# Kernel tuning notes

Hardware: AMD Instinct MI355X
Metric: run time of the kernel (lower is better)

## Reference

```python
import jax, jax.numpy as jnp
import numpy as np

N = 8192
FIN = 128
FOUT = 64
NEG_BIG = -9e15


def setup_inputs() -> dict:
    key = jax.random.key(0)
    k1, k2, k3, k4 = jax.random.split(key, 4)
    x = jax.random.normal(k1, (N, FIN), dtype=jnp.float32)
    adj = jax.random.randint(k2, (N, N), 0, 2, dtype=jnp.int32)
    stdv_w = 1.0 / np.sqrt(FOUT)
    W = jax.random.uniform(k3, (FIN, FOUT), dtype=jnp.float32, minval=-stdv_w, maxval=stdv_w)
    # weight2: stdv = 1/sqrt(1) = 1
    a = jax.random.uniform(k4, (2 * FOUT, 1), dtype=jnp.float32, minval=-1.0, maxval=1.0)
    return {"x": x, "adj": adj, "W": W, "a": a}


def reference(x, adj, W, a):
    # h = x W  -> [N, Fout]
    h = x @ W
    # e_ij = relu(a^T [h_i || h_j]) decomposed exactly: a1.h_i + a2.h_j
    a1 = a[:FOUT, 0]  # [Fout]
    a2 = a[FOUT:, 0]  # [Fout]
    s1 = h @ a1  # [N]
    s2 = h @ a2  # [N]
    e = jax.nn.relu(s1[:, None] + s2[None, :])  # [N, N]
    att_logits = jnp.where(adj > 0, e, jnp.float32(NEG_BIG))
    attention = jax.nn.softmax(att_logits, axis=-1)  # [N, N]
    # dropout omitted (eval mode / p applied only in training)
    out = attention @ h  # [N, Fout]
    return out[None]  # [1, N, Fout] matching batch_size=1 reshape
```

## Files before the change

kernel.cpp:

```cpp
#include <hip/hip_runtime.h>
#include <cstdint>
#include <cstddef>

#define NN 8192
#define FIN 128
#define FOUT 64
#define BM 32
#define BN 64
#define JSPLIT 4
#define JCH (NN / JSPLIT)
#define NCHUNK (JCH / BN)
#define LDP 72

typedef __bf16 bf16x8 __attribute__((ext_vector_type(8)));
typedef unsigned short u16x8 __attribute__((ext_vector_type(8)));
typedef float f32x4 __attribute__((ext_vector_type(4)));

__device__ __forceinline__ unsigned short f2bf(float f) {
    unsigned u = __float_as_uint(f);
    u += 0x7FFFu + ((u >> 16) & 1u);
    return (unsigned short)(u >> 16);
}
__device__ __forceinline__ float bf2f(unsigned short b) {
    return __uint_as_float(((unsigned)b) << 16);
}

__global__ __launch_bounds__(256) void gat_prep(
    const float* __restrict__ x, const float* __restrict__ W,
    const float* __restrict__ a, float* __restrict__ s1,
    float* __restrict__ s2, unsigned short* __restrict__ Ht,
    unsigned int* __restrict__ s2max_enc)
{
    __shared__ __align__(16) float Wt[FOUT][FIN + 4];
    __shared__ float wa1[FIN], wa2[FIN];
    __shared__ float ash[2 * FOUT];
    __shared__ float s2sh[BM];

    const int tid = threadIdx.x;
    const int i0 = blockIdx.x * BM;

    for (int it = 0; it < 32; ++it) {
        int idx = it * 256 + tid;
        int k = idx >> 6, t = idx & 63;
        Wt[t][k] = W[idx];
    }
    if (tid < 2 * FOUT) ash[tid] = a[tid];
    __syncthreads();

    if (tid < FIN) {
        int k = tid;
        float acc = 0.f;
        #pragma unroll 8
        for (int t = 0; t < FOUT; ++t) acc = fmaf(Wt[t][k], ash[t], acc);
        wa1[k] = acc;
    } else {
        int k = tid - FIN;
        float acc = 0.f;
        #pragma unroll 8
        for (int t = 0; t < FOUT; ++t) acc = fmaf(Wt[t][k], ash[FOUT + t], acc);
        wa2[k] = acc;
    }
    __syncthreads();

    {
        int r = tid >> 3;
        int seg = tid & 7;
        const float* xp = x + (size_t)(i0 + r) * FIN + seg * 16;
        float d1 = 0.f, d2 = 0.f;
        #pragma unroll
        for (int m = 0; m < 16; ++m) {
            float xv = xp[m];
            d1 = fmaf(xv, wa1[seg * 16 + m], d1);
            d2 = fmaf(xv, wa2[seg * 16 + m], d2);
        }
        #pragma unroll
        for (int mk = 1; mk < 8; mk <<= 1) {
            d1 += __shfl_xor(d1, mk);
            d2 += __shfl_xor(d2, mk);
        }
        if (seg == 0) {
            s1[i0 + r] = d1;
            s2[i0 + r] = d2;
            s2sh[r] = d2;
        }
    }

    {
        const int lane = tid & 63;
        const int wv = tid >> 6;
        const int ih = wv & 1, nh = wv >> 1;
        const int m = lane & 15, quad = lane >> 4;
        f32x4 hacc0 = {0.f, 0.f, 0.f, 0.f};
        f32x4 hacc1 = {0.f, 0.f, 0.f, 0.f};
        const float* xrow = x + (size_t)(i0 + ih * 16 + m) * FIN + quad * 8;
        #pragma unroll
        for (int ks = 0; ks < 4; ++ks) {
            const float* xp = xrow + ks * 32;
            u16x8 ua;
            #pragma unroll
            for (int jj = 0; jj < 8; ++jj) ua[jj] = f2bf(xp[jj]);
            bf16x8 af = __builtin_bit_cast(bf16x8, ua);
            {
                const float* wp = &Wt[nh * 32 + m][ks * 32 + quad * 8];
                u16x8 ub;
                #pragma unroll
                for (int jj = 0; jj < 8; ++jj) ub[jj] = f2bf(wp[jj]);
                bf16x8 bfr = __builtin_bit_cast(bf16x8, ub);
                hacc0 = __builtin_amdgcn_mfma_f32_16x16x32_bf16(af, bfr, hacc0, 0, 0, 0);
            }
            {
                const float* wp = &Wt[nh * 32 + 16 + m][ks * 32 + quad * 8];
                u16x8 ub;
                #pragma unroll
                for (int jj = 0; jj < 8; ++jj) ub[jj] = f2bf(wp[jj]);
                bf16x8 bfr = __builtin_bit_cast(bf16x8, ub);
                hacc1 = __builtin_amdgcn_mfma_f32_16x16x32_bf16(af, bfr, hacc1, 0, 0, 0);
            }
        }
        #pragma unroll
        for (int reg = 0; reg < 4; ++reg) {
            int irow = i0 + ih * 16 + quad * 4 + reg;
            int t0 = nh * 32 + m;
            Ht[(size_t)t0 * NN + irow] = f2bf(hacc0[reg]);
            Ht[(size_t)(t0 + 16) * NN + irow] = f2bf(hacc1[reg]);
        }
    }
    __syncthreads();
    if (tid == 0) {
        float mx = s2sh[0];
        #pragma unroll
        for (int r = 1; r < BM; ++r) mx = fmaxf(mx, s2sh[r]);
        unsigned ub = __float_as_uint(mx);
        unsigned enc = (ub & 0x80000000u) ? ~ub : (ub | 0x80000000u);
        atomicMax(s2max_enc, enc);
    }
}

__global__ __launch_bounds__(256, 4) void gat_attn(
    const int* __restrict__ adj, const float* __restrict__ s1,
    const float* __restrict__ s2, const unsigned short* __restrict__ Ht,
    const unsigned int* __restrict__ s2max_enc,
    float* __restrict__ pacc, float* __restrict__ pl)
{
    __shared__ __align__(16) unsigned short p_lds[2][BM][LDP];
    __shared__ __align__(16) unsigned short ht_lds[2][FOUT][LDP];
    __shared__ __align__(16) float s2sh[JCH];
    __shared__ float s1v[BM], Mv[BM];

    const int tid = threadIdx.x;
    const int bx = blockIdx.x;
    const int r = bx >> 2;
    const int js = bx & 3;
    const int i0 = r * BM;
    const int j0 = js * JCH;

    const int li = tid >> 4;
    const int jg = (tid & 15) * 4;
    const int th = tid >> 3;
    const int jh = (tid & 7) * 8;

    const int* adjp0 = adj + (size_t)(i0 + li) * NN + j0 + jg;
    const int* adjp1 = adjp0 + 16 * NN;
    const unsigned short* htp0 = Ht + (size_t)th * NN + j0 + jh;
    const unsigned short* htp1 = htp0 + 32 * NN;

    int4 ca0 = *(const int4*)adjp0;
    int4 ca1 = *(const int4*)adjp1;
    uint4 ch0 = *(const uint4*)htp0;
    uint4 ch1 = *(const uint4*)htp1;

    {
        #pragma unroll
        for (int it = 0; it < 2; ++it) {
            int idx = (it * 256 + tid) * 4;
            *(float4*)&s2sh[idx] = *(const float4*)(s2 + j0 + idx);
        }
        unsigned u = *s2max_enc;
        float S2MAX = (u & 0x80000000u) ? __uint_as_float(u ^ 0x80000000u)
                                        : __uint_as_float(~u);
        if (tid < BM) {
            float s = s1[i0 + tid];
            s1v[tid] = s;
            Mv[tid] = fmaxf(0.f, s + S2MAX);
        }
    }
    __syncthreads();

    const int lane = tid & 63;
    const int wv = tid >> 6;
    const int ih = wv & 1, nh = wv >> 1;
    const int cm = lane & 15, quad = lane >> 4;

    f32x4 acc0 = {0.f, 0.f, 0.f, 0.f};
    f32x4 acc1 = {0.f, 0.f, 0.f, 0.f};
    float psA = 0.f, psB = 0.f;

    const float s1a = s1v[li], Ma = Mv[li];
    const float s1b = s1v[li + 16], Mb = Mv[li + 16];

    for (int c = 0; c < NCHUNK; ++c) {
        const int buf = c & 1;

        const int cn = (c + 1 < NCHUNK) ? (c + 1) : c;
        int4 na0 = *(const int4*)(adjp0 + cn * BN);
        int4 na1 = *(const int4*)(adjp1 + cn * BN);
        uint4 nh0 = *(const uint4*)(htp0 + cn * BN);
        uint4 nh1 = *(const uint4*)(htp1 + cn * BN);

        *(uint4*)&ht_lds[buf][th][jh] = ch0;
        *(uint4*)&ht_lds[buf][th + 32][jh] = ch1;

        {
            const int* av0 = (const int*)&ca0;
            const int* av1 = (const int*)&ca1;
            const float* s2v = &s2sh[c * BN + jg];
            unsigned short qa[4], qb[4];
            #pragma unroll
            for (int jj = 0; jj < 4; ++jj) {
                float s2x = s2v[jj];
                float eA = fmaxf(s1a + s2x, 0.f);
                float pA = (av0[jj] > 0) ? __expf(eA - Ma) : 0.f;
                qa[jj] = f2bf(pA);
                psA += bf2f(qa[jj]);
                float eB = fmaxf(s1b + s2x, 0.f);
                float pB = (av1[jj] > 0) ? __expf(eB - Mb) : 0.f;
                qb[jj] = f2bf(pB);
                psB += bf2f(qb[jj]);
            }
            *(ushort4*)&p_lds[buf][li][jg]      = make_ushort4(qa[0], qa[1], qa[2], qa[3]);
            *(ushort4*)&p_lds[buf][li + 16][jg] = make_ushort4(qb[0], qb[1], qb[2], qb[3]);
        }

        __syncthreads();

        #pragma unroll
        for (int ks = 0; ks < 2; ++ks) {
            bf16x8 af  = *(const bf16x8*)&p_lds[buf][ih * 16 + cm][ks * 32 + quad * 8];
            bf16x8 bf0 = *(const bf16x8*)&ht_lds[buf][nh * 32 + cm][ks * 32 + quad * 8];
            bf16x8 bf1 = *(const bf16x8*)&ht_lds[buf][nh * 32 + 16 + cm][ks * 32 + quad * 8];
            acc0 = __builtin_amdgcn_mfma_f32_16x16x32_bf16(af, bf0, acc0, 0, 0, 0);
            acc1 = __builtin_amdgcn_mfma_f32_16x16x32_bf16(af, bf1, acc1, 0, 0, 0);
        }

        ca0 = na0; ca1 = na1; ch0 = nh0; ch1 = nh1;
    }

    #pragma unroll
    for (int mk = 1; mk < 16; mk <<= 1) {
        psA += __shfl_xor(psA, mk);
        psB += __shfl_xor(psB, mk);
    }
    if ((tid & 15) == 0) {
        pl[(size_t)js * NN + i0 + li]      = psA;
        pl[(size_t)js * NN + i0 + li + 16] = psB;
    }

    #pragma unroll
    for (int reg = 0; reg < 4; ++reg) {
        int irow = i0 + ih * 16 + quad * 4 + reg;
        int n0 = nh * 32 + cm;
        pacc[((size_t)js * NN + irow) * FOUT + n0]      = acc0[reg];
        pacc[((size_t)js * NN + irow) * FOUT + n0 + 16] = acc1[reg];
    }
}

__global__ __launch_bounds__(256) void gat_combine(
    const float* __restrict__ pacc, const float* __restrict__ pl,
    float* __restrict__ out)
{
    int idx = blockIdx.x * 256 + threadIdx.x;
    int i = idx >> 6;
    float s = 0.f, l = 0.f;
    #pragma unroll
    for (int js = 0; js < JSPLIT; ++js) {
        s += pacc[(size_t)js * NN * FOUT + idx];
        l += pl[(size_t)js * NN + i];
    }
    out[idx] = s / l;
}

extern "C" void kernel_launch(void* const* d_in, const int* in_sizes, int n_in,
                              void* d_out, int out_size, void* d_ws, size_t ws_size,
                              hipStream_t stream) {
    const float* x   = (const float*)d_in[0];
    const int*   adj = (const int*)d_in[1];
    const float* W   = (const float*)d_in[2];
    const float* a   = (const float*)d_in[3];
    float* out = (float*)d_out;

    char* ws = (char*)d_ws;
    float* s1             = (float*)(ws);
    float* s2             = (float*)(ws + 32768);
    unsigned int* s2enc   = (unsigned int*)(ws + 65536);
    unsigned short* Ht    = (unsigned short*)(ws + 66560);
    float* pacc           = (float*)(ws + 66560 + 1048576);
    float* pl             = (float*)(ws + 66560 + 1048576 + 8388608);

    hipMemsetAsync(s2enc, 0, 4, stream);
    gat_prep<<<NN / BM, 256, 0, stream>>>(x, W, a, s1, s2, Ht, s2enc);
    gat_attn<<<(NN / BM) * JSPLIT, 256, 0, stream>>>(adj, s1, s2, Ht, s2enc, pacc, pl);
    gat_combine<<<NN * FOUT / 256, 256, 0, stream>>>(pacc, pl, out);
}
```

Before: 402.5 us.

## Load Ht MFMA operands directly from global, double J split

Removes the Ht shared-memory staging buffer so each lane reads its bf16 B-fragments for the MFMA straight from global/L2. The change also doubles the column split to 8, which halves per-block work, halves the s2 shared tile and raises occupancy (launch bounds 6). The cost is larger partial accumulators in the workspace, a heavier combine step, and uncoalesced, unprefetched global loads of Ht issued inside the loop.

```diff
diff --git a/kernel.cpp b/kernel.cpp
--- a/kernel.cpp
+++ b/kernel.cpp
@@ -7,7 +7,7 @@
 #define FOUT 64
 #define BM 32
 #define BN 64
-#define JSPLIT 4
+#define JSPLIT 8
 #define JCH (NN / JSPLIT)
 #define NCHUNK (JCH / BN)
 #define LDP 72
@@ -136,45 +136,43 @@
     }
 }
 
-__global__ __launch_bounds__(256, 4) void gat_attn(
+__global__ __launch_bounds__(256, 6) void gat_attn(
     const int* __restrict__ adj, const float* __restrict__ s1,
     const float* __restrict__ s2, const unsigned short* __restrict__ Ht,
     const unsigned int* __restrict__ s2max_enc,
     float* __restrict__ pacc, float* __restrict__ pl)
 {
     __shared__ __align__(16) unsigned short p_lds[2][BM][LDP];
-    __shared__ __align__(16) unsigned short ht_lds[2][FOUT][LDP];
     __shared__ __align__(16) float s2sh[JCH];
     __shared__ float s1v[BM], Mv[BM];
 
     const int tid = threadIdx.x;
     const int bx = blockIdx.x;
-    const int r = bx >> 2;
-    const int js = bx & 3;
+    const int r = bx >> 3;
+    const int js = bx & 7;
     const int i0 = r * BM;
     const int j0 = js * JCH;
 
     const int li = tid >> 4;
     const int jg = (tid & 15) * 4;
-    const int th = tid >> 3;
-    const int jh = (tid & 7) * 8;
 
     const int* adjp0 = adj + (size_t)(i0 + li) * NN + j0 + jg;
     const int* adjp1 = adjp0 + 16 * NN;
-    const unsigned short* htp0 = Ht + (size_t)th * NN + j0 + jh;
-    const unsigned short* htp1 = htp0 + 32 * NN;
 
     int4 ca0 = *(const int4*)adjp0;
     int4 ca1 = *(const int4*)adjp1;
-    uint4 ch0 = *(const uint4*)htp0;
-    uint4 ch1 = *(const uint4*)htp1;
+
+    const int lane = tid & 63;
+    const int wv = tid >> 6;
+    const int ih = wv & 1, nh = wv >> 1;
+    const int cm = lane & 15, quad = lane >> 4;
+
+    const unsigned short* htb0 = Ht + (size_t)(nh * 32 + cm) * NN + j0 + quad * 8;
+    const unsigned short* htb1 = htb0 + (size_t)16 * NN;
 
     {
-        #pragma unroll
-        for (int it = 0; it < 2; ++it) {
-            int idx = (it * 256 + tid) * 4;
-            *(float4*)&s2sh[idx] = *(const float4*)(s2 + j0 + idx);
-        }
+        int idx = tid * 4;
+        *(float4*)&s2sh[idx] = *(const float4*)(s2 + j0 + idx);
         unsigned u = *s2max_enc;
         float S2MAX = (u & 0x80000000u) ? __uint_as_float(u ^ 0x80000000u)
                                         : __uint_as_float(~u);
@@ -186,11 +184,6 @@
     }
     __syncthreads();
 
-    const int lane = tid & 63;
-    const int wv = tid >> 6;
-    const int ih = wv & 1, nh = wv >> 1;
-    const int cm = lane & 15, quad = lane >> 4;
-
     f32x4 acc0 = {0.f, 0.f, 0.f, 0.f};
     f32x4 acc1 = {0.f, 0.f, 0.f, 0.f};
     float psA = 0.f, psB = 0.f;
@@ -201,14 +194,14 @@
     for (int c = 0; c < NCHUNK; ++c) {
         const int buf = c & 1;
 
+        bf16x8 b00 = *(const bf16x8*)(htb0 + c * BN);
+        bf16x8 b01 = *(const bf16x8*)(htb1 + c * BN);
+        bf16x8 b10 = *(const bf16x8*)(htb0 + c * BN + 32);
+        bf16x8 b11 = *(const bf16x8*)(htb1 + c * BN + 32);
+
         const int cn = (c + 1 < NCHUNK) ? (c + 1) : c;
         int4 na0 = *(const int4*)(adjp0 + cn * BN);
         int4 na1 = *(const int4*)(adjp1 + cn * BN);
-        uint4 nh0 = *(const uint4*)(htp0 + cn * BN);
-        uint4 nh1 = *(const uint4*)(htp1 + cn * BN);
-
-        *(uint4*)&ht_lds[buf][th][jh] = ch0;
-        *(uint4*)&ht_lds[buf][th + 32][jh] = ch1;
 
         {
             const int* av0 = (const int*)&ca0;
@@ -233,16 +226,16 @@
 
         __syncthreads();
 
-        #pragma unroll
-        for (int ks = 0; ks < 2; ++ks) {
-            bf16x8 af  = *(const bf16x8*)&p_lds[buf][ih * 16 + cm][ks * 32 + quad * 8];
-            bf16x8 bf0 = *(const bf16x8*)&ht_lds[buf][nh * 32 + cm][ks * 32 + quad * 8];
-            bf16x8 bf1 = *(const bf16x8*)&ht_lds[buf][nh * 32 + 16 + cm][ks * 32 + quad * 8];
-            acc0 = __builtin_amdgcn_mfma_f32_16x16x32_bf16(af, bf0, acc0, 0, 0, 0);
-            acc1 = __builtin_amdgcn_mfma_f32_16x16x32_bf16(af, bf1, acc1, 0, 0, 0);
-        }
-
-        ca0 = na0; ca1 = na1; ch0 = nh0; ch1 = nh1;
+        {
+            bf16x8 af0 = *(const bf16x8*)&p_lds[buf][ih * 16 + cm][quad * 8];
+            bf16x8 af1 = *(const bf16x8*)&p_lds[buf][ih * 16 + cm][32 + quad * 8];
+            acc0 = __builtin_amdgcn_mfma_f32_16x16x32_bf16(af0, b00, acc0, 0, 0, 0);
+            acc1 = __builtin_amdgcn_mfma_f32_16x16x32_bf16(af0, b01, acc1, 0, 0, 0);
+            acc0 = __builtin_amdgcn_mfma_f32_16x16x32_bf16(af1, b10, acc0, 0, 0, 0);
+            acc1 = __builtin_amdgcn_mfma_f32_16x16x32_bf16(af1, b11, acc1, 0, 0, 0);
+        }
+
+        ca0 = na0; ca1 = na1;
     }
 
     #pragma unroll
@@ -294,7 +287,7 @@
     unsigned int* s2enc   = (unsigned int*)(ws + 65536);
     unsigned short* Ht    = (unsigned short*)(ws + 66560);
     float* pacc           = (float*)(ws + 66560 + 1048576);
-    float* pl             = (float*)(ws + 66560 + 1048576 + 8388608);
+    float* pl             = (float*)(ws + 66560 + 1048576 + 16777216);
 
     hipMemsetAsync(s2enc, 0, 4, stream);
     gat_prep<<<NN / BM, 256, 0, stream>>>(x, W, a, s1, s2, Ht, s2enc);
```

New measurement: 402.1 us. About the same (-0.1%).
